# Kernel tuning notes

Hardware: AMD Instinct MI355X
Metric: run time of the kernel (lower is better)

Reference implementation:

```python
import jax, jax.numpy as jnp
import numpy as np

B, S, J, D = 64, 2048, 25, 3
FEAT_DIM = 128
COMPUTED = 12  # pos(3) + vel(3) + acc(3) + angles(3)
IN_MLP = COMPUTED * J  # 300
HID = FEAT_DIM * 2     # 256
CONN = np.array([(0, 1), (1, 5), (1, 6), (5, 7), (7, 9), (6, 8), (8, 10),
                 (1, 11), (1, 12), (11, 13), (13, 15), (12, 14), (14, 16)], dtype=np.int32)


def setup_inputs() -> dict:
    key = jax.random.key(0)
    ks = jax.random.split(key, 8)
    return {
        "poses": jax.random.normal(ks[0], (B, S, J, D), dtype=jnp.float32),
        "W1": jax.random.normal(ks[1], (IN_MLP, HID), dtype=jnp.float32) * 0.05,
        "b1": jnp.zeros((HID,), jnp.float32),
        "gamma": jnp.ones((HID,), jnp.float32),
        "beta": jnp.zeros((HID,), jnp.float32),
        "running_mean": jnp.zeros((HID,), jnp.float32),
        "running_var": jnp.ones((HID,), jnp.float32),
        "W2": jax.random.normal(ks[2], (HID, FEAT_DIM), dtype=jnp.float32) * 0.05,
        "b2": jnp.zeros((FEAT_DIM,), jnp.float32),
        "joint_weights": jnp.ones((J,), jnp.float32),
    }


def reference(poses, W1, b1, gamma, beta, running_mean, running_var, W2, b2, joint_weights):
    b, s, j, d = poses.shape
    # --- root-centering + max-distance normalization ---
    p = poses - poses[:, :, 0:1, :]
    dist = jnp.linalg.norm(p, axis=-1, keepdims=True)           # [B,S,J,1]
    max_dist = jnp.max(dist, axis=2, keepdims=True)             # [B,S,1,1]
    p = p / (max_dist + 1e-8)
    # --- velocity / acceleration (zero-padded first frames) ---
    zpad = jnp.zeros_like(p[:, :1])
    vel = jnp.concatenate([zpad, p[:, 1:] - p[:, :-1]], axis=1)
    acc = jnp.concatenate([zpad, vel[:, 1:] - vel[:, :-1]], axis=1)
    # --- joint angles: vectorized gather + normalize + acos (replaces B*S*13 python loop) ---
    v1 = p[:, :, CONN[:, 1], :] - p[:, :, CONN[:, 0], :]        # [B,S,13,3]
    vnorm = jnp.maximum(jnp.linalg.norm(v1, axis=-1, keepdims=True), 1e-12)  # F.normalize eps
    ang = jnp.arccos(jnp.clip(v1 / vnorm, -1.0, 1.0))           # [B,S,13,3]
    ang = ang.reshape(b, s, -1)                                 # [B,S,39]
    pad = jnp.zeros((b, s, j * 3 - ang.shape[-1]), ang.dtype)   # pad to J*3=75
    angles = jnp.concatenate([ang, pad], axis=-1).reshape(b, s, j, 3)
    # --- combine, weight, project ---
    feat = jnp.concatenate([p, vel, acc, angles], axis=-1)      # [B,S,J,12]
    feat = feat * joint_weights.reshape(1, 1, j, 1)
    x = feat.reshape(b * s, -1)                                 # [B*S,300]
    x = x @ W1 + b1
    x = gamma * (x - running_mean) / jnp.sqrt(running_var + 1e-5) + beta  # BN eval mode
    x = jax.nn.relu(x)                                          # dropout = identity (eval)
    x = x @ W2 + b2
    return x.reshape(b, s, -1)                                  # [B,S,128]
```

## Files before the change

kernel.cpp:

```cpp
#include <hip/hip_runtime.h>
#include <stdint.h>


#define S_    2048
#define MT_   64
#define TPB   512
#define HID_  256
#define OUT_  128
#define NTOK  131072
#define F_    66

typedef __attribute__((ext_vector_type(8))) _Float16 half8;
typedef __attribute__((ext_vector_type(4))) float    floatx4;
typedef __attribute__((ext_vector_type(4))) float    f4_t;

#define C0M 0x0ECDB118675110ULL
#define C1M 0x0FDECBA9786540ULL

__device__ __forceinline__ float facos(float x) {
    float ax = fabsf(x);
    float p = fmaf(ax, -0.0187293f, 0.0742610f);
    p = fmaf(ax, p, -0.2121144f);
    p = fmaf(ax, p, 1.5707288f);
    float r = __builtin_amdgcn_sqrtf(1.f - ax) * p;
    return x < 0.f ? 3.14159265358979f - r : r;
}

__global__ void prep_kernel(const float* __restrict__ W1, const float* __restrict__ b1,
                            const float* __restrict__ gamma, const float* __restrict__ beta,
                            const float* __restrict__ rmean, const float* __restrict__ rvar,
                            const float* __restrict__ W2, const float* __restrict__ jw,
                            _Float16* __restrict__ w1p,
                            _Float16* __restrict__ w2p,
                            float* __restrict__ b1p) {
    int bid = blockIdx.x, tid = threadIdx.x;
    if (bid < 352) {
        int k = bid, n = tid;
        float a = gamma[n] * __builtin_amdgcn_rsqf(rvar[n] + 1e-5f);
        float v = 0.f;
        if (k < 288) {
            int d = k / 96, loc = k - d * 96;
            if (loc < 75) {
                int j = loc / 3, c = loc - j * 3;
                const float* Wb = W1 + (j * 12 + c) * HID_ + n;
                float wp = Wb[0], wv = Wb[3 * HID_], wa = Wb[6 * HID_];
                float t = (d == 0) ? (wp + wv + wa) : (d == 1 ? -(wv + 2.f * wa) : wa);
                v = t * a * jw[j];
            }
        } else {
            int q = k - 288;
            if (q < 39) {
                int e = q / 3, aa = q - e * 3;
                v = W1[(e * 12 + 9 + aa) * HID_ + n] * a * jw[e];
            }
        }
        int blk = (k >> 5) * 16 + (n >> 4);
        int off = blk * 512 + (((k >> 3) & 3) * 16 + (n & 15)) * 8 + (k & 7);
        w1p[off] = (_Float16)v;
    } else if (bid < 480) {
        int i2 = (bid - 352) * 256 + tid;
        int k = i2 >> 7, n = i2 & 127;
        int blk = (k >> 5) * 8 + (n >> 4);
        int off = blk * 512 + (((k >> 3) & 3) * 16 + (n & 15)) * 8 + (k & 7);
        w2p[off] = (_Float16)W2[k * OUT_ + n];
    } else {
        int n = tid;
        float a = gamma[n] * __builtin_amdgcn_rsqf(rvar[n] + 1e-5f);
        b1p[n] = fmaf(a, b1[n] - rmean[n], beta[n]);
    }
}

#define L_CCB 0
#define L_AB  11632
#define L_RAW 16800
#define L_RS  36608
#define L_TOT 37696

__global__ __launch_bounds__(TPB, 6) void pose_mlp(
    const float* __restrict__ poses,
    const _Float16* __restrict__ w1p,
    const _Float16* __restrict__ w2p,
    const float* __restrict__ b1p,
    const float* __restrict__ b2,
    float* __restrict__ out)
{
    __shared__ __align__(16) unsigned char smem[L_TOT];
    const int tid  = threadIdx.x;
    const int lane = tid & 63;
    const int wv   = tid >> 6;
    const int t0   = blockIdx.x * MT_;
    const int s0   = t0 & (S_ - 1);

    _Float16* ccb = (_Float16*)(smem + L_CCB);
    _Float16* ab  = (_Float16*)(smem + L_AB);
    float*    raw = (float*)(smem + L_RAW);
    float4*   rs  = (float4*)(smem + L_RS);

    half8 bw[2];
    #pragma unroll
    for (int ni = 0; ni < 2; ni++)
        bw[ni] = *(const half8*)(w1p + (unsigned)(wv * 2 + ni) * 512 + lane * 8);
    float bv[2];
    #pragma unroll
    for (int ni = 0; ni < 2; ni++) bv[ni] = b1p[wv * 32 + ni * 16 + (lane & 15)];
    float c2 = b2[wv * 16 + (lane & 15)];

    if (tid < 152) {
        int src = t0 * 75 - 150 + tid;
        if (s0 == 0) { if (tid < 75) src += 150; else if (tid < 150) src += 75; }
        raw[tid] = poses[src];
    }
    {
        const float2* ps = (const float2*)(poses + (size_t)t0 * 75 + 2);
        #pragma unroll 1
        for (int i = tid; i < 2399; i += TPB) {
            float2 v = ps[i];
            *(float2*)(raw + 152 + 2 * i) = v;
        }
    }
    if (tid < 96) {
        if (tid < 8)       ccb[F_ * 88 + tid] = (_Float16)0.f;
        else if (tid < 32) ab[MT_ * 40 + (tid - 8)] = (_Float16)0.f;
        else               ab[(tid - 32) * 40 + 39] = (_Float16)0.f;
    }
    __syncthreads();

    #pragma unroll
    for (int r2 = 0; r2 < 2; r2++) {
        int i = r2 * TPB + tid;
        int tt = i >> 4, e = i & 15;
        if (e < 13) {
            const float* R = raw + (tt + 2) * 75;
            int a0 = (int)((C0M >> (4 * e)) & 15) * 3;
            int a1 = (((int)((C1M >> (4 * e)) & 15)) + 1) * 3;
            float vx = R[a1] - R[a0], vy = R[a1 + 1] - R[a0 + 1], vz = R[a1 + 2] - R[a0 + 2];
            float d  = fmaf(vx, vx, fmaf(vy, vy, vz * vz));
            float inv = __builtin_amdgcn_rcpf(fmaxf(__builtin_amdgcn_sqrtf(d), 1e-12f));
            _Float16* A = ab + tt * 40;
            A[e * 3 + 0] = (_Float16)facos(fminf(fmaxf(vx * inv, -1.f), 1.f));
            A[e * 3 + 1] = (_Float16)facos(fminf(fmaxf(vy * inv, -1.f), 1.f));
            A[e * 3 + 2] = (_Float16)facos(fminf(fmaxf(vz * inv, -1.f), 1.f));
        }
    }
    if (tid < F_ * 4) {
        int f = tid >> 2, q = tid & 3;
        const float* R = raw + f * 75;
        float r0 = R[0], r1 = R[1], r2 = R[2];
        float m2 = 0.f;
        #pragma unroll
        for (int jj = 0; jj < 7; jj++) {
            int j = q * 7 + jj;
            if (j < 25) {
                float dx = R[j * 3]     - r0;
                float dy = R[j * 3 + 1] - r1;
                float dz = R[j * 3 + 2] - r2;
                m2 = fmaxf(m2, fmaf(dx, dx, fmaf(dy, dy, dz * dz)));
            }
        }
        m2 = fmaxf(m2, __shfl_xor(m2, 1));
        m2 = fmaxf(m2, __shfl_xor(m2, 2));
        if (q == 0) {
            float sc = __builtin_amdgcn_rcpf(__builtin_amdgcn_sqrtf(m2) + 1e-8f);
            rs[f] = make_float4(r0, r1, r2, sc);
        }
    }
    __syncthreads();

    #pragma unroll 1
    for (int i = tid; i < F_ * 32; i += TPB) {
        int f = i >> 5, j = i & 31;
        _Float16* C = ccb + f * 88;
        if (j < 25) {
            const float* R = raw + f * 75 + j * 3;
            float4 q = rs[f];
            C[j * 3 + 0] = (_Float16)((R[0] - q.x) * q.w);
            C[j * 3 + 1] = (_Float16)((R[1] - q.y) * q.w);
            C[j * 3 + 2] = (_Float16)((R[2] - q.z) * q.w);
        } else {
            int c = 75 + (j - 25) * 2;
            C[c] = (_Float16)0.f;
            if (c + 1 < 88) C[c + 1] = (_Float16)0.f;
        }
    }
    __syncthreads();

    floatx4 acc[4][2];
    #pragma unroll
    for (int mi = 0; mi < 4; mi++)
        #pragma unroll
        for (int ni = 0; ni < 2; ni++)
            acc[mi][ni] = (floatx4){bv[ni], bv[ni], bv[ni], bv[ni]};

    int rowb[4];
    #pragma unroll
    for (int mi = 0; mi < 4; mi++)
        rowb[mi] = (mi * 16 + (lane & 15) + 2) * 88 + (lane >> 4) * 8;

    int koff = 0;
    #pragma unroll 1
    for (int kc = 0; kc < 9; kc++) {
        half8 bn[2];
        #pragma unroll
        for (int ni = 0; ni < 2; ni++)
            bn[ni] = *(const half8*)(w1p + (unsigned)((kc + 1) * 16 + wv * 2 + ni) * 512 + lane * 8);
        half8 af[4];
        #pragma unroll
        for (int mi = 0; mi < 4; mi++)
            af[mi] = *(const half8*)(ccb + rowb[mi] + koff);
        #pragma unroll
        for (int mi = 0; mi < 4; mi++)
            #pragma unroll
            for (int ni = 0; ni < 2; ni++)
                acc[mi][ni] = __builtin_amdgcn_mfma_f32_16x16x32_f16(
                    af[mi], bw[ni], acc[mi][ni], 0, 0, 0);
        bw[0] = bn[0]; bw[1] = bn[1];
        koff += 32; if (kc == 2 || kc == 5) koff -= 184;
    }
    {
        int rowa[4];
        #pragma unroll
        for (int mi = 0; mi < 4; mi++)
            rowa[mi] = (mi * 16 + (lane & 15)) * 40 + (lane >> 4) * 8;
        #pragma unroll
        for (int kc = 9; kc < 11; kc++) {
            half8 bn[2];
            if (kc < 10) {
                #pragma unroll
                for (int ni = 0; ni < 2; ni++)
                    bn[ni] = *(const half8*)(w1p + (unsigned)((kc + 1) * 16 + wv * 2 + ni) * 512 + lane * 8);
            }
            half8 af[4];
            #pragma unroll
            for (int mi = 0; mi < 4; mi++)
                af[mi] = *(const half8*)(ab + rowa[mi] + (kc - 9) * 32);
            #pragma unroll
            for (int mi = 0; mi < 4; mi++)
                #pragma unroll
                for (int ni = 0; ni < 2; ni++)
                    acc[mi][ni] = __builtin_amdgcn_mfma_f32_16x16x32_f16(
                        af[mi], bw[ni], acc[mi][ni], 0, 0, 0);
            if (kc < 10) { bw[0] = bn[0]; bw[1] = bn[1]; }
        }
    }

    half8 bw2 = *(const half8*)(w2p + (unsigned)wv * 512 + lane * 8);

    __syncthreads();

    _Float16* hid = (_Float16*)smem;
    #pragma unroll
    for (int mi = 0; mi < 4; mi++)
        #pragma unroll
        for (int ni = 0; ni < 2; ni++)
            #pragma unroll
            for (int r = 0; r < 4; r++) {
                float v = fmaxf(acc[mi][ni][r], 0.f);
                int m   = mi * 16 + (lane >> 4) * 4 + r;
                int col = wv * 32 + ni * 16 + (lane & 15);
                hid[m * 264 + col] = (_Float16)v;
            }
    __syncthreads();

    floatx4 acc2[4];
    #pragma unroll
    for (int mi = 0; mi < 4; mi++) acc2[mi] = (floatx4){c2, c2, c2, c2};

    #pragma unroll 1
    for (int kc = 0; kc < 8; kc++) {
        half8 bn2;
        if (kc < 7)
            bn2 = *(const half8*)(w2p + (unsigned)((kc + 1) * 8 + wv) * 512 + lane * 8);
        half8 af[4];
        #pragma unroll
        for (int mi = 0; mi < 4; mi++)
            af[mi] = *(const half8*)(hid + (mi * 16 + (lane & 15)) * 264 + kc * 32 + (lane >> 4) * 8);
        #pragma unroll
        for (int mi = 0; mi < 4; mi++)
            acc2[mi] = __builtin_amdgcn_mfma_f32_16x16x32_f16(
                af[mi], bw2, acc2[mi], 0, 0, 0);
        if (kc < 7) bw2 = bn2;
    }
    __syncthreads();

    float* obuf = (float*)smem;
    #pragma unroll
    for (int mi = 0; mi < 4; mi++)
        #pragma unroll
        for (int r = 0; r < 4; r++) {
            int m = mi * 16 + (lane >> 4) * 4 + r;
            obuf[m * 132 + wv * 16 + (lane & 15)] = acc2[mi][r];
        }
    __syncthreads();
    #pragma unroll
    for (int k = 0; k < 4; k++) {
        int idx = k * TPB + tid;
        int row = idx >> 5, c4 = idx & 31;
        f4_t v = *(const f4_t*)(obuf + row * 132 + c4 * 4);
        __builtin_nontemporal_store(v, (f4_t*)out + (size_t)t0 * 32 + idx);
    }
}

extern "C" void kernel_launch(void* const* d_in, const int* in_sizes, int n_in,
                              void* d_out, int out_size, void* d_ws, size_t ws_size,
                              hipStream_t stream) {
    (void)in_sizes; (void)n_in; (void)out_size; (void)ws_size;
    const float* poses = (const float*)d_in[0];
    const float* W1    = (const float*)d_in[1];
    const float* b1    = (const float*)d_in[2];
    const float* gamma = (const float*)d_in[3];
    const float* beta  = (const float*)d_in[4];
    const float* rmean = (const float*)d_in[5];
    const float* rvar  = (const float*)d_in[6];
    const float* W2    = (const float*)d_in[7];
    const float* b2    = (const float*)d_in[8];
    const float* jw    = (const float*)d_in[9];

    _Float16* w1p = (_Float16*)d_ws;
    _Float16* w2p = w1p + 352 * HID_;
    float* b1p = (float*)((char*)d_ws + (352 * HID_ + HID_ * OUT_) * 2);

    prep_kernel<<<481, 256, 0, stream>>>(W1, b1, gamma, beta, rmean, rvar, W2, jw,
                                         w1p, w2p, b1p);
    pose_mlp<<<2048, TPB, 0, stream>>>(poses, w1p, w2p, b1p, b2, (float*)d_out);
}
```

Before: 162.8 us.

## Read poses directly from global memory and store output without LDS staging

Removes the shared-memory staging buffer for raw poses and has the angle, max-distance and normalization stages read poses straight from global memory, relying on cache. It also drops the LDS transpose of the output so each lane writes scalar floats directly, which removes two barriers, and raises the launch-bounds occupancy hint from 6 to 8 blocks per CU since LDS use shrinks. The trade-off is repeated uncoalesced global loads of poses, scalar rather than vectorized non-temporal output stores, and more register pressure from the tighter occupancy bound.

```diff
diff --git a/kernel.cpp b/kernel.cpp
--- a/kernel.cpp
+++ b/kernel.cpp
@@ -7,12 +7,9 @@
 #define TPB   512
 #define HID_  256
 #define OUT_  128
-#define NTOK  131072
-#define F_    66
 
 typedef __attribute__((ext_vector_type(8))) _Float16 half8;
 typedef __attribute__((ext_vector_type(4))) float    floatx4;
-typedef __attribute__((ext_vector_type(4))) float    f4_t;
 
 #define C0M 0x0ECDB118675110ULL
 #define C1M 0x0FDECBA9786540ULL
@@ -72,11 +69,10 @@
 
 #define L_CCB 0
 #define L_AB  11632
-#define L_RAW 16800
-#define L_RS  36608
-#define L_TOT 37696
-
-__global__ __launch_bounds__(TPB, 6) void pose_mlp(
+#define L_RS  16800
+#define L_TOT 33792
+
+__global__ __launch_bounds__(TPB, 8) void pose_mlp(
     const float* __restrict__ poses,
     const _Float16* __restrict__ w1p,
     const _Float16* __restrict__ w2p,
@@ -93,7 +89,6 @@
 
     _Float16* ccb = (_Float16*)(smem + L_CCB);
     _Float16* ab  = (_Float16*)(smem + L_AB);
-    float*    raw = (float*)(smem + L_RAW);
     float4*   rs  = (float4*)(smem + L_RS);
 
     half8 bw[2];
@@ -105,35 +100,21 @@
     for (int ni = 0; ni < 2; ni++) bv[ni] = b1p[wv * 32 + ni * 16 + (lane & 15)];
     float c2 = b2[wv * 16 + (lane & 15)];
 
-    if (tid < 152) {
-        int src = t0 * 75 - 150 + tid;
-        if (s0 == 0) { if (tid < 75) src += 150; else if (tid < 150) src += 75; }
-        raw[tid] = poses[src];
-    }
-    {
-        const float2* ps = (const float2*)(poses + (size_t)t0 * 75 + 2);
-        #pragma unroll 1
-        for (int i = tid; i < 2399; i += TPB) {
-            float2 v = ps[i];
-            *(float2*)(raw + 152 + 2 * i) = v;
-        }
-    }
     if (tid < 96) {
-        if (tid < 8)       ccb[F_ * 88 + tid] = (_Float16)0.f;
-        else if (tid < 32) ab[MT_ * 40 + (tid - 8)] = (_Float16)0.f;
+        if (tid < 8)       ccb[66 * 88 + tid] = (_Float16)0.f;
+        else if (tid < 32) ab[64 * 40 + (tid - 8)] = (_Float16)0.f;
         else               ab[(tid - 32) * 40 + 39] = (_Float16)0.f;
     }
-    __syncthreads();
 
     #pragma unroll
     for (int r2 = 0; r2 < 2; r2++) {
         int i = r2 * TPB + tid;
         int tt = i >> 4, e = i & 15;
         if (e < 13) {
-            const float* R = raw + (tt + 2) * 75;
+            const float* P = poses + (size_t)(t0 + tt) * 75;
             int a0 = (int)((C0M >> (4 * e)) & 15) * 3;
             int a1 = (((int)((C1M >> (4 * e)) & 15)) + 1) * 3;
-            float vx = R[a1] - R[a0], vy = R[a1 + 1] - R[a0 + 1], vz = R[a1 + 2] - R[a0 + 2];
+            float vx = P[a1] - P[a0], vy = P[a1+1] - P[a0+1], vz = P[a1+2] - P[a0+2];
             float d  = fmaf(vx, vx, fmaf(vy, vy, vz * vz));
             float inv = __builtin_amdgcn_rcpf(fmaxf(__builtin_amdgcn_sqrtf(d), 1e-12f));
             _Float16* A = ab + tt * 40;
@@ -142,18 +123,21 @@
             A[e * 3 + 2] = (_Float16)facos(fminf(fmaxf(vz * inv, -1.f), 1.f));
         }
     }
-    if (tid < F_ * 4) {
+
+    if (tid < 264) {
         int f = tid >> 2, q = tid & 3;
-        const float* R = raw + f * 75;
-        float r0 = R[0], r1 = R[1], r2 = R[2];
+        int g = t0 + f - 2;
+        if (s0 == 0 && f < 2) g = t0;
+        const float* P = poses + (size_t)g * 75;
+        float r0 = P[0], r1 = P[1], r2 = P[2];
         float m2 = 0.f;
         #pragma unroll
         for (int jj = 0; jj < 7; jj++) {
             int j = q * 7 + jj;
             if (j < 25) {
-                float dx = R[j * 3]     - r0;
-                float dy = R[j * 3 + 1] - r1;
-                float dz = R[j * 3 + 2] - r2;
+                float dx = P[j*3]   - r0;
+                float dy = P[j*3+1] - r1;
+                float dz = P[j*3+2] - r2;
                 m2 = fmaxf(m2, fmaf(dx, dx, fmaf(dy, dy, dz * dz)));
             }
         }
@@ -167,15 +151,17 @@
     __syncthreads();
 
     #pragma unroll 1
-    for (int i = tid; i < F_ * 32; i += TPB) {
+    for (int i = tid; i < 66 * 32; i += TPB) {
         int f = i >> 5, j = i & 31;
         _Float16* C = ccb + f * 88;
         if (j < 25) {
-            const float* R = raw + f * 75 + j * 3;
+            int g = t0 + f - 2;
+            if (s0 == 0 && f < 2) g = t0;
+            const float* P = poses + (size_t)g * 75 + j * 3;
             float4 q = rs[f];
-            C[j * 3 + 0] = (_Float16)((R[0] - q.x) * q.w);
-            C[j * 3 + 1] = (_Float16)((R[1] - q.y) * q.w);
-            C[j * 3 + 2] = (_Float16)((R[2] - q.z) * q.w);
+            C[j * 3 + 0] = (_Float16)((P[0] - q.x) * q.w);
+            C[j * 3 + 1] = (_Float16)((P[1] - q.y) * q.w);
+            C[j * 3 + 2] = (_Float16)((P[2] - q.z) * q.w);
         } else {
             int c = 75 + (j - 25) * 2;
             C[c] = (_Float16)0.f;
@@ -280,24 +266,15 @@
                 af[mi], bw2, acc2[mi], 0, 0, 0);
         if (kc < 7) bw2 = bn2;
     }
-    __syncthreads();
-
-    float* obuf = (float*)smem;
+
     #pragma unroll
     for (int mi = 0; mi < 4; mi++)
         #pragma unroll
         for (int r = 0; r < 4; r++) {
-            int m = mi * 16 + (lane >> 4) * 4 + r;
-            obuf[m * 132 + wv * 16 + (lane & 15)] = acc2[mi][r];
-        }
-    __syncthreads();
-    #pragma unroll
-    for (int k = 0; k < 4; k++) {
-        int idx = k * TPB + tid;
-        int row = idx >> 5, c4 = idx & 31;
-        f4_t v = *(const f4_t*)(obuf + row * 132 + c4 * 4);
-        __builtin_nontemporal_store(v, (f4_t*)out + (size_t)t0 * 32 + idx);
-    }
+            int m   = mi * 16 + (lane >> 4) * 4 + r;
+            int col = wv * 16 + (lane & 15);
+            out[(size_t)(t0 + m) * OUT_ + col] = acc2[mi][r];
+        }
 }
 
 extern "C" void kernel_launch(void* const* d_in, const int* in_sizes, int n_in,
```

Result: faster. 147.2 us (-9.6%).
